# Kernel optimization log

Measured on AMD Instinct MI355X. Metric: run time of the kernel, lower is better.

The kernel has to match this reference:

```python
import jax, jax.numpy as jnp
import numpy as np

N_HEADS = 8; DH = 64; G = 4; K = 9
C = N_HEADS * DH; CG = C // G
FACTOR = 2.0; TAU = 1.0
SCALE = DH ** -0.5


def _conv1x1(x, w, b):
    # x: (C, *spatial), w: (O, C), b: (O,)
    y = jnp.tensordot(w, x, axes=([1], [0]))
    return y + b.reshape((-1,) + (1,) * (y.ndim - 1))


def _dwconv(x, w, b):
    # depthwise 3x3, SAME padding; x (N,Cg,H,W), w (Cg,1,3,3)
    y = jax.lax.conv_general_dilated(x, w, (1, 1), 'SAME',
                                     feature_group_count=x.shape[1],
                                     dimension_numbers=('NCHW', 'OIHW', 'NCHW'))
    return y + b[None, :, None, None]


def _ln(x, g, b):
    # LayerNormProxy: LN over channel dim of NCHW (torch default eps=1e-5)
    m = jnp.mean(x, axis=1, keepdims=True)
    v = jnp.var(x, axis=1, keepdims=True)
    return (x - m) / jnp.sqrt(v + 1e-5) * g[None, :, None, None] + b[None, :, None, None]


def _grid_sample(img, grid):
    # bilinear, align_corners=True, padding_mode='zeros'
    # img (N,C,H,W), grid (N,Hg,Wg,2) with (x,y) in [-1,1]
    N, Cc, H, W = img.shape
    gx = (grid[..., 0] + 1.0) * 0.5 * (W - 1)
    gy = (grid[..., 1] + 1.0) * 0.5 * (H - 1)
    x0 = jnp.floor(gx); y0 = jnp.floor(gy)

    def g(yy, xx):
        yi = jnp.clip(yy, 0, H - 1).astype(jnp.int32)
        xi = jnp.clip(xx, 0, W - 1).astype(jnp.int32)
        ok = ((yy >= 0) & (yy <= H - 1) & (xx >= 0) & (xx <= W - 1)).astype(img.dtype)
        vals = jax.vmap(lambda im, a, b: im[:, a, b])(img, yi, xi)  # (N,C,Hg,Wg)
        return vals * ok[:, None]

    wx1 = gx - x0; wx0 = 1.0 - wx1
    wy1 = gy - y0; wy0 = 1.0 - wy1
    return (g(y0, x0) * (wy0 * wx0)[:, None]
            + g(y0, x0 + 1) * (wy0 * wx1)[:, None]
            + g(y0 + 1, x0) * (wy1 * wx0)[:, None]
            + g(y0 + 1, x0 + 1) * (wy1 * wx1)[:, None])


def _forward(x, idx, labels, wq, bq, wk, bk, wv, bv, wo, bo,
             ow1, ob1, g1, b1, ow2, ob2, g2, b2, ow3):
    _, _, H, W = x.shape
    n = idx.shape[0]
    iy, ix = idx[:, 0], idx[:, 1]

    q = _conv1x1(x[0], wq, bq)[None]               # (1,C,H,W)
    q_off = q.reshape(G, CG, H, W)                 # (b g) c h w with b=1
    q_sel = q[0][:, iy, ix]                        # (C,n)

    # offset predictor: dwconv -> LN -> GELU (x2) -> 1x1 (no bias)
    t = jax.nn.gelu(_ln(_dwconv(q_off, ow1, ob1), g1, b1), approximate=False)
    t = jax.nn.gelu(_ln(_dwconv(t, ow2, ob2), g2, b2), approximate=False)
    offset = jnp.einsum('gchw,oc->gohw', t, ow3)   # (G,2K,H,W)

    # offset_range_factor > 0: tanh * [1/H,1/W] (tiled K times) * factor
    rng = jnp.tile(jnp.array([1.0 / H, 1.0 / W], offset.dtype), K)
    offset = jnp.tanh(offset) * rng[None, :, None, None] * FACTOR
    off = offset.transpose(0, 2, 3, 1).reshape(G, H, W, K, 2)  # (g,h,w,K,(y,x))

    # reference points in [-1,1] (y,x), unfolded over 3x3 window w/ replication pad
    ry = (jnp.arange(H, dtype=x.dtype) + 0.5) / H * 2.0 - 1.0
    rx = (jnp.arange(W, dtype=x.dtype) + 0.5) / W * 2.0 - 1.0
    ref = jnp.stack(jnp.meshgrid(ry, rx, indexing='ij'), 0)    # (2,H,W)
    pad = jnp.pad(ref, ((0, 0), (1, 1), (1, 1)), mode='edge')
    patches = jnp.stack([pad[:, dy:dy + H, dx:dx + W]
                         for dy in range(3) for dx in range(3)], 0)  # (K,2,H,W)
    ref_unf = patches.transpose(2, 3, 0, 1)                    # (H,W,K,2)

    pos = off + ref_unf[None]                                  # (G,H,W,K,2)
    pos = pos.transpose(0, 3, 1, 2, 4).reshape(G * K, H, W, 2)
    grid = pos[..., ::-1]                                      # (x,y) order

    # gather per-group channels at K learned locations per position
    xg = x.reshape(G, CG, H, W)
    img = jnp.broadcast_to(xg[:, None], (G, K, CG, H, W)).reshape(G * K, CG, H, W)
    xs = _grid_sample(img, grid)                               # (GK,CG,H,W)
    xs = xs.reshape(G, K, CG, H, W).transpose(0, 2, 1, 3, 4).reshape(C, K, H, W)
    xs_sel = xs[:, :, iy, ix]                                  # (C,K,n)

    k = _conv1x1(xs_sel, wk, bk).reshape(N_HEADS, DH, K, n).transpose(0, 1, 3, 2)  # (h,d,n,K)
    v = _conv1x1(xs_sel, wv, bv).reshape(N_HEADS, DH, K, n).transpose(0, 1, 3, 2)
    qh = q_sel.reshape(N_HEADS, DH, n)

    attn = jnp.einsum('hdn,hdnk->hnk', qh, k) * SCALE
    attn = jax.nn.softmax(attn / TAU, axis=-1)                 # (h,n,K)
    out = jnp.einsum('hnk,hdnk->hdn', attn, v).reshape(C, n)
    y = _conv1x1(out, wo, bo).T                                # (n, dim_out)

    sig = jax.nn.sigmoid(y[jnp.arange(n), labels])

    # second grid_sample over full channels at the same learned positions
    img_full = jnp.broadcast_to(x, (G * K, C, H, W))
    xr = _grid_sample(img_full, grid)                          # (GK,C,H,W)
    xr_sel = xr[:, :, iy, ix].transpose(2, 0, 1)               # (n,GK,C)
    return y, attn, xr_sel, sig


def setup_inputs() -> dict:
    key = jax.random.key(0)
    ks = jax.random.split(key, 16)
    H = W = 64; n = 2048; s = 0.02
    return dict(
        x=jax.random.normal(ks[0], (1, C, H, W), jnp.float32),
        idx=jax.random.randint(ks[1], (n, 2), 0, H),
        labels=jax.random.randint(ks[2], (n,), 0, C),
        wq=jax.random.normal(ks[3], (C, C), jnp.float32) * s, bq=jnp.zeros((C,), jnp.float32),
        wk=jax.random.normal(ks[4], (C, C), jnp.float32) * s, bk=jnp.zeros((C,), jnp.float32),
        wv=jax.random.normal(ks[5], (C, C), jnp.float32) * s, bv=jnp.zeros((C,), jnp.float32),
        wo=jax.random.normal(ks[6], (C, C), jnp.float32) * s, bo=jnp.zeros((C,), jnp.float32),
        ow1=jax.random.normal(ks[7], (CG, 1, 3, 3), jnp.float32) * s, ob1=jnp.zeros((CG,), jnp.float32),
        g1=jnp.ones((CG,), jnp.float32), b1=jnp.zeros((CG,), jnp.float32),
        ow2=jax.random.normal(ks[8], (CG, 1, 3, 3), jnp.float32) * s, ob2=jnp.zeros((CG,), jnp.float32),
        g2=jnp.ones((CG,), jnp.float32), b2=jnp.zeros((CG,), jnp.float32),
        ow3=jax.random.normal(ks[9], (2 * K, CG), jnp.float32) * s,
    )


def reference(x, idx, labels, wq, bq, wk, bk, wv, bv, wo, bo,
              ow1, ob1, g1, b1, ow2, ob2, g2, b2, ow3):
    return _forward(x, idx, labels, wq, bq, wk, bk, wv, bv, wo, bo,
                    ow1, ob1, g1, b1, ow2, ob2, g2, b2, ow3)
```

## Files before the change

### kernel.cpp

```cpp
#include <hip/hip_runtime.h>
#include <math.h>

namespace {

typedef unsigned short u16;
typedef unsigned int u32;
typedef __attribute__((ext_vector_type(8))) short bf16x8;
typedef __attribute__((ext_vector_type(4))) float f32x4;
typedef __attribute__((ext_vector_type(2))) float f32x2;
typedef __attribute__((ext_vector_type(2))) unsigned int u32x2;

constexpr int HDIM = 64;
constexpr int WDIM = 64;
constexpr int HW = HDIM * WDIM;
constexpr int C = 512;
constexpr int G = 4;
constexpr int CG = 128;
constexpr int K = 9;
constexpr int NH = 8;
constexpr float SCALE = 0.125f;

__device__ __forceinline__ u16 f2b(float f) {
  union { float f; u32 u; } v; v.f = f;
  u32 u = v.u;
  return (u16)((u + 0x7FFFu + ((u >> 16) & 1u)) >> 16);
}
__device__ __forceinline__ float b2f(u16 b) {
  union { u32 u; float f; } v; v.u = ((u32)b) << 16;
  return v.f;
}

__global__ void __launch_bounds__(256)
k_prep(const float* __restrict__ wq, const float* __restrict__ wv,
       const float* __restrict__ wo, const float* __restrict__ wk,
       const float* __restrict__ x,
       u16* __restrict__ wqb, u16* __restrict__ wvb, u16* __restrict__ wob,
       u16* __restrict__ wkT, u16* __restrict__ xtb) {
  int b = blockIdx.x;
  int t = threadIdx.x;
  if (b < 1024) {
    int j = b * 256 + t;
    wqb[j] = f2b(wq[j]);
    wvb[j] = f2b(wv[j]);
    wob[j] = f2b(wo[j]);
    return;
  }
  __shared__ float tile[32][33];
  int tx = t & 31, ty = t >> 5;
  if (b < 1280) {
    int bb = b - 1024;
    int r0 = (bb & 15) * 32, c0 = (bb >> 4) * 32;
    for (int r = ty; r < 32; r += 8) tile[r][tx] = wk[(r0 + r) * C + c0 + tx];
    __syncthreads();
    for (int r = ty; r < 32; r += 8) wkT[(c0 + r) * C + r0 + tx] = f2b(tile[tx][r]);
  } else {
    int bb = b - 1280;
    int p0 = (bb & 127) * 32, c0 = (bb >> 7) * 32;
    for (int r = ty; r < 32; r += 8) tile[r][tx] = x[(c0 + r) * HW + p0 + tx];
    __syncthreads();
    for (int r = ty; r < 32; r += 8) xtb[(p0 + r) * C + c0 + tx] = f2b(tile[tx][r]);
  }
}

template <bool OUT_BF16>
__global__ void __launch_bounds__(256)
k_gemm_mfma(const u16* __restrict__ A, int lda, int aOffZ,
            const int* __restrict__ aIdx,
            const u16* __restrict__ BT, int ldb, int bOffZ,
            const float* __restrict__ bias, int biasOffZ,
            void* __restrict__ Dp, int ldd, int dOffZ, int Kd,
            const int* __restrict__ labels, float* __restrict__ sigp) {
  int z = blockIdx.z;
  const u16* Ab = A + (size_t)z * aOffZ;
  const u16* Bb = BT + (size_t)z * bOffZ;
  int t = threadIdx.x;
  int wave = t >> 6, lane = t & 63;
  int wm = (wave >> 1) * 32, wn = (wave & 1) * 32;
  int bm = blockIdx.x * 64 + wm;
  int bn = blockIdx.y * 64 + wn;
  int row = lane & 15, quad = lane >> 4;
  size_t ar[2];
#pragma unroll
  for (int mt = 0; mt < 2; ++mt) {
    int r = bm + mt * 16 + row;
    ar[mt] = aIdx ? (size_t)(aIdx[2 * r] * WDIM + aIdx[2 * r + 1]) : (size_t)r;
  }
  f32x4 acc[2][2] = {};
  for (int k0 = 0; k0 < Kd; k0 += 32) {
    bf16x8 a[2], b[2];
#pragma unroll
    for (int mt = 0; mt < 2; ++mt)
      a[mt] = *(const bf16x8*)&Ab[ar[mt] * lda + k0 + quad * 8];
#pragma unroll
    for (int nt = 0; nt < 2; ++nt)
      b[nt] = *(const bf16x8*)&Bb[(size_t)(bn + nt * 16 + row) * ldb + k0 + quad * 8];
#pragma unroll
    for (int mt = 0; mt < 2; ++mt)
#pragma unroll
      for (int nt = 0; nt < 2; ++nt)
        acc[mt][nt] = __builtin_amdgcn_mfma_f32_16x16x32_bf16(a[mt], b[nt], acc[mt][nt], 0, 0, 0);
  }
#pragma unroll
  for (int nt = 0; nt < 2; ++nt) {
    int cc = bn + nt * 16 + row;
    float bb = bias ? bias[(size_t)z * biasOffZ + cc] : 0.0f;
#pragma unroll
    for (int mt = 0; mt < 2; ++mt)
#pragma unroll
      for (int r = 0; r < 4; ++r) {
        int rr = bm + mt * 16 + quad * 4 + r;
        float v = acc[mt][nt][r] + bb;
        if (OUT_BF16) {
          ((u16*)Dp)[(size_t)z * dOffZ + (size_t)rr * ldd + cc] = f2b(v);
        } else {
          ((float*)Dp)[(size_t)z * dOffZ + (size_t)rr * ldd + cc] = v;
          if (labels && labels[rr] == cc) sigp[rr] = 1.0f / (1.0f + expf(-v));
        }
      }
  }
}

__global__ void __launch_bounds__(256)
k_mix(const u16* __restrict__ q_tb, const float* __restrict__ w9,
      const float* __restrict__ wb, const float* __restrict__ lng,
      const float* __restrict__ lnb, u16* __restrict__ t1b,
      const u16* __restrict__ wkT, const int* __restrict__ idx,
      u16* __restrict__ qk2b) {
  int b = blockIdx.x;
  int t = threadIdx.x;
  if (b < HW) {
    int p = b;
    int h = p >> 6, w = p & 63;
    int c0 = t * 2;
    int cg0 = c0 & 127, cg1 = cg0 + 1;
    float a0 = wb[cg0], a1 = wb[cg1];
#pragma unroll
    for (int dy = 0; dy < 3; ++dy) {
      int hh = h + dy - 1;
      if (hh < 0 || hh >= HDIM) continue;
#pragma unroll
      for (int dx = 0; dx < 3; ++dx) {
        int ww = w + dx - 1;
        if (ww < 0 || ww >= WDIM) continue;
        u32 pr2 = *(const u32*)&q_tb[(hh * WDIM + ww) * C + c0];
        float wt0 = w9[cg0 * 9 + dy * 3 + dx];
        float wt1 = w9[cg1 * 9 + dy * 3 + dx];
        a0 += wt0 * b2f((u16)pr2);
        a1 += wt1 * b2f((u16)(pr2 >> 16));
      }
    }
    float s = a0 + a1, s2 = a0 * a0 + a1 * a1;
#pragma unroll
    for (int o = 32; o > 0; o >>= 1) {
      s += __shfl_xor(s, o, 64);
      s2 += __shfl_xor(s2, o, 64);
    }
    float mean = s * (1.0f / 128.0f);
    float var = s2 * (1.0f / 128.0f) - mean * mean;
    float rstd = rsqrtf(var + 1e-5f);
    float xn0 = (a0 - mean) * rstd * lng[cg0] + lnb[cg0];
    float xn1 = (a1 - mean) * rstd * lng[cg1] + lnb[cg1];
    u16 o0 = f2b(0.5f * xn0 * (1.0f + erff(xn0 * 0.70710678f)));
    u16 o1 = f2b(0.5f * xn1 * (1.0f + erff(xn1 * 0.70710678f)));
    *(u32*)&t1b[(size_t)p * C + c0] = ((u32)o1 << 16) | o0;
  } else {
    int bb = b - HW;
    int m = bb & 31, nn = (bb >> 5) & 7, z = bb >> 8;
    const u16* Ab = q_tb + z * 64;
    const u16* Bb = wkT + z * 64;
    int wave = t >> 6, lane = t & 63;
    int wm = (wave >> 1) * 32, wn = (wave & 1) * 32;
    int bm = m * 64 + wm;
    int bn = nn * 64 + wn;
    int row = lane & 15, quad = lane >> 4;
    size_t ar[2];
#pragma unroll
    for (int mt = 0; mt < 2; ++mt) {
      int r = bm + mt * 16 + row;
      ar[mt] = (size_t)(idx[2 * r] * WDIM + idx[2 * r + 1]);
    }
    f32x4 acc[2][2] = {};
#pragma unroll
    for (int k0 = 0; k0 < 64; k0 += 32) {
      bf16x8 a[2], bfr[2];
#pragma unroll
      for (int mt = 0; mt < 2; ++mt)
        a[mt] = *(const bf16x8*)&Ab[ar[mt] * C + k0 + quad * 8];
#pragma unroll
      for (int nt = 0; nt < 2; ++nt)
        bfr[nt] = *(const bf16x8*)&Bb[(size_t)(bn + nt * 16 + row) * C + k0 + quad * 8];
#pragma unroll
      for (int mt = 0; mt < 2; ++mt)
#pragma unroll
        for (int nt = 0; nt < 2; ++nt)
          acc[mt][nt] = __builtin_amdgcn_mfma_f32_16x16x32_bf16(a[mt], bfr[nt], acc[mt][nt], 0, 0, 0);
    }
#pragma unroll
    for (int nt = 0; nt < 2; ++nt) {
      int cc = bn + nt * 16 + row;
#pragma unroll
      for (int mt = 0; mt < 2; ++mt)
#pragma unroll
        for (int r = 0; r < 4; ++r) {
          int rr = bm + mt * 16 + quad * 4 + r;
          qk2b[(size_t)rr * (NH * C) + z * C + cc] = f2b(acc[mt][nt][r]);
        }
    }
  }
}

__global__ void __launch_bounds__(256)
k_attn6(const u16* __restrict__ t1, const float* __restrict__ w9,
        const float* __restrict__ wb, const float* __restrict__ lng,
        const float* __restrict__ lnb, const float* __restrict__ ow3,
        const int* __restrict__ idx,
        const u16* __restrict__ qk2b, const u16* __restrict__ xtb,
        float* __restrict__ attn_out, u16* __restrict__ z2b,
        float* __restrict__ xr, int n) {
  constexpr int LD = 520;
  int i = blockIdx.x;
  int t = threadIdx.x;
  __shared__ alignas(16) u16 qkl[8 * LD];
  __shared__ alignas(16) u16 xsl[16 * LD];
  __shared__ int ro[36][4];
  __shared__ float wbl[36][4];
  __shared__ float lg[NH][K];
  int wave = t >> 6, lane = t & 63;
  int iy = idx[2 * i], ix = idx[2 * i + 1];
  {
    const bf16x8* qs = (const bf16x8*)(qk2b + (size_t)i * (NH * C));
#pragma unroll
    for (int cix = t; cix < 512; cix += 256) {
      bf16x8 val = qs[cix];
      int r = cix >> 6;
      int co = (cix & 63) * 8;
      *(bf16x8*)&qkl[r * LD + co] = val;
    }
  }
  {
    int c0 = t * 2;
    int cg0 = c0 & 127, cg1 = cg0 + 1;
    int g = wave;
    float a0 = wb[cg0], a1 = wb[cg1];
#pragma unroll
    for (int dy = 0; dy < 3; ++dy) {
      int hh = iy + dy - 1;
      if (hh < 0 || hh >= HDIM) continue;
#pragma unroll
      for (int dx = 0; dx < 3; ++dx) {
        int ww = ix + dx - 1;
        if (ww < 0 || ww >= WDIM) continue;
        u32 pr2 = *(const u32*)&t1[(hh * WDIM + ww) * C + c0];
        float wt0 = w9[cg0 * 9 + dy * 3 + dx];
        float wt1 = w9[cg1 * 9 + dy * 3 + dx];
        a0 += wt0 * b2f((u16)pr2);
        a1 += wt1 * b2f((u16)(pr2 >> 16));
      }
    }
    float s = a0 + a1, s2 = a0 * a0 + a1 * a1;
#pragma unroll
    for (int o = 32; o > 0; o >>= 1) {
      s += __shfl_xor(s, o, 64);
      s2 += __shfl_xor(s2, o, 64);
    }
    float mean = s * (1.0f / 128.0f);
    float var = s2 * (1.0f / 128.0f) - mean * mean;
    float rstd = rsqrtf(var + 1e-5f);
    float xn0 = (a0 - mean) * rstd * lng[cg0] + lnb[cg0];
    float xn1 = (a1 - mean) * rstd * lng[cg1] + lnb[cg1];
    float x0 = 0.5f * xn0 * (1.0f + erff(xn0 * 0.70710678f));
    float x1 = 0.5f * xn1 * (1.0f + erff(xn1 * 0.70710678f));
    float ovreg = 0.0f;
#pragma unroll
    for (int l = 0; l < 18; ++l) {
      float a = ow3[l * CG + cg0] * x0 + ow3[l * CG + cg1] * x1;
#pragma unroll
      for (int o = 32; o > 0; o >>= 1) a += __shfl_xor(a, o, 64);
      if (lane == l) ovreg = a;
    }
    int ls = (lane < 9) ? lane : 0;
    float vy = __shfl(ovreg, 2 * ls, 64);
    float vx = __shfl(ovreg, 2 * ls + 1, 64);
    if (lane < 9) {
      int dy = lane / 3, dx = lane % 3;
      int ryi = min(max(iy + dy - 1, 0), HDIM - 1);
      int rxi = min(max(ix + dx - 1, 0), WDIM - 1);
      float ry = (ryi + 0.5f) * (2.0f / HDIM) - 1.0f;
      float rx = (rxi + 0.5f) * (2.0f / WDIM) - 1.0f;
      float py = tanhf(vy) * (2.0f / HDIM) + ry;
      float px = tanhf(vx) * (2.0f / WDIM) + rx;
      int it = g * 9 + lane;
      float gx = (px + 1.0f) * 0.5f * (WDIM - 1);
      float gy = (py + 1.0f) * 0.5f * (HDIM - 1);
      float x0f = floorf(gx), y0f = floorf(gy);
      float wx1 = gx - x0f, wx0 = 1.0f - wx1;
      float wy1 = gy - y0f, wy0 = 1.0f - wy1;
      int bx0 = (int)x0f, by0 = (int)y0f;
      int bx1 = bx0 + 1, by1 = by0 + 1;
      bool vx0 = (bx0 >= 0) && (bx0 < WDIM);
      bool vx1b = (bx1 >= 0) && (bx1 < WDIM);
      bool vy0 = (by0 >= 0) && (by0 < HDIM);
      bool vy1b = (by1 >= 0) && (by1 < HDIM);
      wbl[it][0] = (vy0 && vx0) ? wy0 * wx0 : 0.0f;
      wbl[it][1] = (vy0 && vx1b) ? wy0 * wx1 : 0.0f;
      wbl[it][2] = (vy1b && vx0) ? wy1 * wx0 : 0.0f;
      wbl[it][3] = (vy1b && vx1b) ? wy1 * wx1 : 0.0f;
      int x0c = min(max(bx0, 0), WDIM - 1), x1c = min(max(bx1, 0), WDIM - 1);
      int y0c = min(max(by0, 0), HDIM - 1), y1c = min(max(by1, 0), HDIM - 1);
      ro[it][0] = (y0c * WDIM + x0c) * C;
      ro[it][1] = (y0c * WDIM + x1c) * C;
      ro[it][2] = (y1c * WDIM + x0c) * C;
      ro[it][3] = (y1c * WDIM + x1c) * C;
    }
  }
  __syncthreads();
  float* xrb = xr + (size_t)i * (G * K) * C;
  {
    int half = t >> 7;
    int th = t & 127;
    int c4 = th * 4;
#pragma unroll 3
    for (int j = 0; j < 18; ++j) {
      int it = 2 * j + half;
      float w00 = wbl[it][0], w01 = wbl[it][1], w10 = wbl[it][2], w11 = wbl[it][3];
      u32x2 q00 = *(const u32x2*)&xtb[ro[it][0] + c4];
      u32x2 q01 = *(const u32x2*)&xtb[ro[it][1] + c4];
      u32x2 q10 = *(const u32x2*)&xtb[ro[it][2] + c4];
      u32x2 q11 = *(const u32x2*)&xtb[ro[it][3] + c4];
      float v0 = w00 * b2f((u16)q00.x) + w01 * b2f((u16)q01.x) +
                 w10 * b2f((u16)q10.x) + w11 * b2f((u16)q11.x);
      float v1 = w00 * b2f((u16)(q00.x >> 16)) + w01 * b2f((u16)(q01.x >> 16)) +
                 w10 * b2f((u16)(q10.x >> 16)) + w11 * b2f((u16)(q11.x >> 16));
      float v2 = w00 * b2f((u16)q00.y) + w01 * b2f((u16)q01.y) +
                 w10 * b2f((u16)q10.y) + w11 * b2f((u16)q11.y);
      float v3 = w00 * b2f((u16)(q00.y >> 16)) + w01 * b2f((u16)(q01.y >> 16)) +
                 w10 * b2f((u16)(q10.y >> 16)) + w11 * b2f((u16)(q11.y >> 16));
      f32x4 ov = {v0, v1, v2, v3};
      __builtin_nontemporal_store(ov, (f32x4*)&xrb[(size_t)it * C + c4]);
      int gi = (it * 57) >> 9;
      if ((th >> 5) == gi) {
        int kk = it - gi * 9;
        u32x2 pk;
        pk.x = ((u32)f2b(v1) << 16) | f2b(v0);
        pk.y = ((u32)f2b(v3) << 16) | f2b(v2);
        *(u32x2*)&xsl[kk * LD + c4] = pk;
      }
    }
  }
  __syncthreads();
  if (wave == 0) {
    int row = lane & 15, quad = lane >> 4;
    f32x4 acc = {};
    __builtin_amdgcn_s_setprio(1);
#pragma unroll 4
    for (int k0 = 0; k0 < C; k0 += 32) {
      bf16x8 a = *(const bf16x8*)&qkl[(row & 7) * LD + k0 + quad * 8];
      bf16x8 b = *(const bf16x8*)&xsl[row * LD + k0 + quad * 8];
      acc = __builtin_amdgcn_mfma_f32_16x16x32_bf16(a, b, acc, 0, 0, 0);
    }
    __builtin_amdgcn_s_setprio(0);
    if (row < K && quad < 2) {
#pragma unroll
      for (int r = 0; r < 4; ++r) lg[quad * 4 + r][row] = acc[r] * SCALE;
    }
  }
  __syncthreads();
  {
    u16* zrow = z2b + (size_t)i * (NH * C);
#pragma unroll
    for (int hh = 0; hh < 2; ++hh) {
      int h = wave * 2 + hh;
      float mx = -1e30f;
#pragma unroll
      for (int kk = 0; kk < K; ++kk) mx = fmaxf(mx, lg[h][kk]);
      float e[K];
      float sm = 0.0f;
#pragma unroll
      for (int kk = 0; kk < K; ++kk) { e[kk] = expf(lg[h][kk] - mx); sm += e[kk]; }
      float inv = 1.0f / sm;
      if (lane < K) attn_out[((size_t)h * n + i) * K + lane] = e[lane] * inv;
      float accz[8] = {};
#pragma unroll
      for (int kk = 0; kk < K; ++kk) {
        bf16x8 v = *(const bf16x8*)&xsl[kk * LD + lane * 8];
        float p = e[kk] * inv;
#pragma unroll
        for (int el = 0; el < 8; ++el) accz[el] += p * b2f((u16)v[el]);
      }
      u16 ob[8];
#pragma unroll
      for (int el = 0; el < 8; ++el) ob[el] = f2b(accz[el]);
      *(bf16x8*)&zrow[h * C + lane * 8] = *(const bf16x8*)ob;
    }
  }
}

}

extern "C" void kernel_launch(void* const* d_in, const int* in_sizes, int n_in,
                              void* d_out, int out_size, void* d_ws, size_t ws_size,
                              hipStream_t stream) {
  (void)n_in; (void)out_size; (void)ws_size;
  const float* x = (const float*)d_in[0];
  const int* idx = (const int*)d_in[1];
  const int* labels = (const int*)d_in[2];
  const float* wq = (const float*)d_in[3];
  const float* bq = (const float*)d_in[4];
  const float* wk = (const float*)d_in[5];
  const float* wv = (const float*)d_in[7];
  const float* bv = (const float*)d_in[8];
  const float* wo = (const float*)d_in[9];
  const float* bo = (const float*)d_in[10];
  const float* ow1 = (const float*)d_in[11];
  const float* ob1 = (const float*)d_in[12];
  const float* g1 = (const float*)d_in[13];
  const float* b1 = (const float*)d_in[14];
  const float* ow2 = (const float*)d_in[15];
  const float* ob2 = (const float*)d_in[16];
  const float* g2 = (const float*)d_in[17];
  const float* b2 = (const float*)d_in[18];
  const float* ow3 = (const float*)d_in[19];
  int n = in_sizes[1] / 2;

  unsigned char* wp = (unsigned char*)d_ws;
  auto alloc = [&](size_t bytes) {
    unsigned char* p = wp;
    wp += (bytes + 255) & ~(size_t)255;
    return p;
  };
  u16* xtb = (u16*)alloc((size_t)HW * C * 2);
  u16* wqb = (u16*)alloc((size_t)C * C * 2);
  u16* wvb = (u16*)alloc((size_t)C * C * 2);
  u16* wob = (u16*)alloc((size_t)C * C * 2);
  u16* wkT = (u16*)alloc((size_t)C * C * 2);
  u16* q_tb = (u16*)alloc((size_t)HW * C * 2);
  u16* t1b = (u16*)alloc((size_t)HW * C * 2);
  u16* qk2b = (u16*)alloc((size_t)n * NH * C * 2);
  u16* z2b = (u16*)alloc((size_t)n * NH * C * 2);
  u16* outb = (u16*)alloc((size_t)n * C * 2);

  float* out_f = (float*)d_out;
  float* y_out = out_f;
  float* attn_out = y_out + (size_t)n * C;
  float* xr_out = attn_out + (size_t)NH * n * K;
  float* sig_out = xr_out + (size_t)n * G * K * C;

  k_prep<<<dim3(3328), 256, 0, stream>>>(wq, wv, wo, wk, x, wqb, wvb, wob, wkT, xtb);

  k_gemm_mfma<true><<<dim3(HW / 64, C / 64, 1), 256, 0, stream>>>(
      xtb, C, 0, nullptr, wqb, C, 0, bq, 0, q_tb, C, 0, C, nullptr, nullptr);

  k_mix<<<dim3(HW + 2048), 256, 0, stream>>>(q_tb, ow1, ob1, g1, b1, t1b, wkT, idx, qk2b);

  k_attn6<<<dim3(n), 256, 0, stream>>>(t1b, ow2, ob2, g2, b2, ow3, idx,
                                       qk2b, xtb, attn_out, z2b, xr_out, n);

  k_gemm_mfma<true><<<dim3(n / 64, 1, NH), 256, 0, stream>>>(
      z2b, NH * C, C, nullptr, wvb, C, 64 * C, bv, 64, outb, C, 64, C, nullptr, nullptr);

  k_gemm_mfma<false><<<dim3(n / 64, C / 64, 1), 256, 0, stream>>>(
      outb, C, 0, nullptr, wob, C, 0, bo, 0, y_out, C, 0, C, labels, sig_out);
}
```

Before: 299.6 us.

## Keep sampling coords in registers and compute logits redundantly per wave

Bilinear sample weights and offsets now stay in registers and reach the other lanes by wave shuffles, so each wave gathers its own group's 9 points with 8-wide loads. The shared-memory tables and their barrier are gone. Every wave now runs the small QK MFMA itself and pulls its heads' logits by shuffle, which removes the logit shared array and two more barriers. The cost is four times the MFMA work and a different gather access pattern.

```diff
diff --git a/kernel.cpp b/kernel.cpp
--- a/kernel.cpp
+++ b/kernel.cpp
@@ -210,7 +210,7 @@
 }
 
 __global__ void __launch_bounds__(256)
-k_attn6(const u16* __restrict__ t1, const float* __restrict__ w9,
+k_attn7(const u16* __restrict__ t1, const float* __restrict__ w9,
         const float* __restrict__ wb, const float* __restrict__ lng,
         const float* __restrict__ lnb, const float* __restrict__ ow3,
         const int* __restrict__ idx,
@@ -222,9 +222,6 @@
   int t = threadIdx.x;
   __shared__ alignas(16) u16 qkl[8 * LD];
   __shared__ alignas(16) u16 xsl[16 * LD];
-  __shared__ int ro[36][4];
-  __shared__ float wbl[36][4];
-  __shared__ float lg[NH][K];
   int wave = t >> 6, lane = t & 63;
   int iy = idx[2 * i], ix = idx[2 * i + 1];
   {
@@ -232,15 +229,14 @@
 #pragma unroll
     for (int cix = t; cix < 512; cix += 256) {
       bf16x8 val = qs[cix];
-      int r = cix >> 6;
-      int co = (cix & 63) * 8;
-      *(bf16x8*)&qkl[r * LD + co] = val;
-    }
-  }
+      *(bf16x8*)&qkl[(cix >> 6) * LD + (cix & 63) * 8] = val;
+    }
+  }
+  float tw00 = 0.0f, tw01 = 0.0f, tw10 = 0.0f, tw11 = 0.0f;
+  int tr0 = 0, tr1 = 0, tr2 = 0, tr3 = 0;
   {
     int c0 = t * 2;
     int cg0 = c0 & 127, cg1 = cg0 + 1;
-    int g = wave;
     float a0 = wb[cg0], a1 = wb[cg1];
 #pragma unroll
     for (int dy = 0; dy < 3; ++dy) {
@@ -289,7 +285,6 @@
       float rx = (rxi + 0.5f) * (2.0f / WDIM) - 1.0f;
       float py = tanhf(vy) * (2.0f / HDIM) + ry;
       float px = tanhf(vx) * (2.0f / WDIM) + rx;
-      int it = g * 9 + lane;
       float gx = (px + 1.0f) * 0.5f * (WDIM - 1);
       float gy = (py + 1.0f) * 0.5f * (HDIM - 1);
       float x0f = floorf(gx), y0f = floorf(gy);
@@ -301,54 +296,52 @@
       bool vx1b = (bx1 >= 0) && (bx1 < WDIM);
       bool vy0 = (by0 >= 0) && (by0 < HDIM);
       bool vy1b = (by1 >= 0) && (by1 < HDIM);
-      wbl[it][0] = (vy0 && vx0) ? wy0 * wx0 : 0.0f;
-      wbl[it][1] = (vy0 && vx1b) ? wy0 * wx1 : 0.0f;
-      wbl[it][2] = (vy1b && vx0) ? wy1 * wx0 : 0.0f;
-      wbl[it][3] = (vy1b && vx1b) ? wy1 * wx1 : 0.0f;
+      tw00 = (vy0 && vx0) ? wy0 * wx0 : 0.0f;
+      tw01 = (vy0 && vx1b) ? wy0 * wx1 : 0.0f;
+      tw10 = (vy1b && vx0) ? wy1 * wx0 : 0.0f;
+      tw11 = (vy1b && vx1b) ? wy1 * wx1 : 0.0f;
       int x0c = min(max(bx0, 0), WDIM - 1), x1c = min(max(bx1, 0), WDIM - 1);
       int y0c = min(max(by0, 0), HDIM - 1), y1c = min(max(by1, 0), HDIM - 1);
-      ro[it][0] = (y0c * WDIM + x0c) * C;
-      ro[it][1] = (y0c * WDIM + x1c) * C;
-      ro[it][2] = (y1c * WDIM + x0c) * C;
-      ro[it][3] = (y1c * WDIM + x1c) * C;
+      tr0 = (y0c * WDIM + x0c) * C;
+      tr1 = (y0c * WDIM + x1c) * C;
+      tr2 = (y1c * WDIM + x0c) * C;
+      tr3 = (y1c * WDIM + x1c) * C;
+    }
+  }
+  {
+    int c8 = lane * 8;
+    bool own = (lane >> 4) == wave;
+    float* xrb = xr + ((size_t)i * (G * K) + wave * 9) * C;
+#pragma unroll 3
+    for (int kk = 0; kk < K; ++kk) {
+      float w00 = __shfl(tw00, kk, 64), w01 = __shfl(tw01, kk, 64);
+      float w10 = __shfl(tw10, kk, 64), w11 = __shfl(tw11, kk, 64);
+      int r0 = __shfl(tr0, kk, 64), r1 = __shfl(tr1, kk, 64);
+      int r2 = __shfl(tr2, kk, 64), r3 = __shfl(tr3, kk, 64);
+      bf16x8 q00 = *(const bf16x8*)&xtb[r0 + c8];
+      bf16x8 q01 = *(const bf16x8*)&xtb[r1 + c8];
+      bf16x8 q10 = *(const bf16x8*)&xtb[r2 + c8];
+      bf16x8 q11 = *(const bf16x8*)&xtb[r3 + c8];
+      float v[8];
+#pragma unroll
+      for (int e = 0; e < 8; ++e)
+        v[e] = w00 * b2f((u16)q00[e]) + w01 * b2f((u16)q01[e]) +
+               w10 * b2f((u16)q10[e]) + w11 * b2f((u16)q11[e]);
+      f32x4 lo = {v[0], v[1], v[2], v[3]};
+      f32x4 hi = {v[4], v[5], v[6], v[7]};
+      float* dst = &xrb[(size_t)kk * C + c8];
+      __builtin_nontemporal_store(lo, (f32x4*)dst);
+      __builtin_nontemporal_store(hi, (f32x4*)(dst + 4));
+      if (own) {
+        u16 pk[8];
+#pragma unroll
+        for (int e = 0; e < 8; ++e) pk[e] = f2b(v[e]);
+        *(bf16x8*)&xsl[kk * LD + c8] = *(const bf16x8*)pk;
+      }
     }
   }
   __syncthreads();
-  float* xrb = xr + (size_t)i * (G * K) * C;
   {
-    int half = t >> 7;
-    int th = t & 127;
-    int c4 = th * 4;
-#pragma unroll 3
-    for (int j = 0; j < 18; ++j) {
-      int it = 2 * j + half;
-      float w00 = wbl[it][0], w01 = wbl[it][1], w10 = wbl[it][2], w11 = wbl[it][3];
-      u32x2 q00 = *(const u32x2*)&xtb[ro[it][0] + c4];
-      u32x2 q01 = *(const u32x2*)&xtb[ro[it][1] + c4];
-      u32x2 q10 = *(const u32x2*)&xtb[ro[it][2] + c4];
-      u32x2 q11 = *(const u32x2*)&xtb[ro[it][3] + c4];
-      float v0 = w00 * b2f((u16)q00.x) + w01 * b2f((u16)q01.x) +
-                 w10 * b2f((u16)q10.x) + w11 * b2f((u16)q11.x);
-      float v1 = w00 * b2f((u16)(q00.x >> 16)) + w01 * b2f((u16)(q01.x >> 16)) +
-                 w10 * b2f((u16)(q10.x >> 16)) + w11 * b2f((u16)(q11.x >> 16));
-      float v2 = w00 * b2f((u16)q00.y) + w01 * b2f((u16)q01.y) +
-                 w10 * b2f((u16)q10.y) + w11 * b2f((u16)q11.y);
-      float v3 = w00 * b2f((u16)(q00.y >> 16)) + w01 * b2f((u16)(q01.y >> 16)) +
-                 w10 * b2f((u16)(q10.y >> 16)) + w11 * b2f((u16)(q11.y >> 16));
-      f32x4 ov = {v0, v1, v2, v3};
-      __builtin_nontemporal_store(ov, (f32x4*)&xrb[(size_t)it * C + c4]);
-      int gi = (it * 57) >> 9;
-      if ((th >> 5) == gi) {
-        int kk = it - gi * 9;
-        u32x2 pk;
-        pk.x = ((u32)f2b(v1) << 16) | f2b(v0);
-        pk.y = ((u32)f2b(v3) << 16) | f2b(v2);
-        *(u32x2*)&xsl[kk * LD + c4] = pk;
-      }
-    }
-  }
-  __syncthreads();
-  if (wave == 0) {
     int row = lane & 15, quad = lane >> 4;
     f32x4 acc = {};
     __builtin_amdgcn_s_setprio(1);
@@ -359,24 +352,22 @@
       acc = __builtin_amdgcn_mfma_f32_16x16x32_bf16(a, b, acc, 0, 0, 0);
     }
     __builtin_amdgcn_s_setprio(0);
-    if (row < K && quad < 2) {
-#pragma unroll
-      for (int r = 0; r < 4; ++r) lg[quad * 4 + r][row] = acc[r] * SCALE;
-    }
-  }
-  __syncthreads();
-  {
+    int srcbase = (wave >> 1) << 4;
     u16* zrow = z2b + (size_t)i * (NH * C);
 #pragma unroll
     for (int hh = 0; hh < 2; ++hh) {
       int h = wave * 2 + hh;
+      float av = (wave & 1) ? acc[hh + 2] : acc[hh];
+      float lgv[K];
+#pragma unroll
+      for (int kk = 0; kk < K; ++kk) lgv[kk] = __shfl(av, srcbase + kk, 64) * SCALE;
       float mx = -1e30f;
 #pragma unroll
-      for (int kk = 0; kk < K; ++kk) mx = fmaxf(mx, lg[h][kk]);
+      for (int kk = 0; kk < K; ++kk) mx = fmaxf(mx, lgv[kk]);
       float e[K];
       float sm = 0.0f;
 #pragma unroll
-      for (int kk = 0; kk < K; ++kk) { e[kk] = expf(lg[h][kk] - mx); sm += e[kk]; }
+      for (int kk = 0; kk < K; ++kk) { e[kk] = expf(lgv[kk] - mx); sm += e[kk]; }
       float inv = 1.0f / sm;
       if (lane < K) attn_out[((size_t)h * n + i) * K + lane] = e[lane] * inv;
       float accz[8] = {};
@@ -452,7 +443,7 @@
 
   k_mix<<<dim3(HW + 2048), 256, 0, stream>>>(q_tb, ow1, ob1, g1, b1, t1b, wkT, idx, qk2b);
 
-  k_attn6<<<dim3(n), 256, 0, stream>>>(t1b, ow2, ob2, g2, b2, ow3, idx,
+  k_attn7<<<dim3(n), 256, 0, stream>>>(t1b, ow2, ob2, g2, b2, ow3, idx,
                                        qk2b, xtb, attn_out, z2b, xr_out, n);
 
   k_gemm_mfma<true><<<dim3(n / 64, 1, NH), 256, 0, stream>>>(
```

New measurement: 306.8 us. 1.02x slower.
